# Performance work log

Measured on AMD Instinct MI355X. Metric: run time of the kernel, lower is better.

The kernel has to match this reference:

```python
import jax, jax.numpy as jnp
import numpy as np

H2 = 512  # 2 * hidden_dim
B, TK = 64, 2048


def setup_inputs() -> dict:
    key = jax.random.key(0)
    ks = jax.random.split(key, 10)
    s_t_hat = jax.random.normal(ks[0], (B, H2), dtype=jnp.float32)
    encoder_outputs = jax.random.normal(ks[1], (B, TK, H2), dtype=jnp.float32)
    encoder_feature = jax.random.normal(ks[2], (B, TK, H2), dtype=jnp.float32)
    enc_padding_mask = jnp.ones((B, TK), dtype=jnp.float32)
    coverage = jax.random.uniform(ks[3], (B, TK), dtype=jnp.float32)
    # learned params (torch Linear stores W as [out, in]; we keep math explicit)
    sc = 1.0 / np.sqrt(H2)
    W_dp = jax.random.uniform(ks[4], (H2, H2), minval=-sc, maxval=sc, dtype=jnp.float32)  # decode_proj weight [out,in]
    b_dp = jax.random.uniform(ks[5], (H2,), minval=-sc, maxval=sc, dtype=jnp.float32)
    W_c = jax.random.uniform(ks[6], (H2,), minval=-1.0, maxval=1.0, dtype=jnp.float32)  # Linear(1, 2H) weight, squeezed
    v_w = jax.random.uniform(ks[7], (H2,), minval=-sc, maxval=sc, dtype=jnp.float32)  # Linear(2H, 1) weight
    v_b = jax.random.uniform(ks[8], (), minval=-sc, maxval=sc, dtype=jnp.float32)
    return {
        "s_t_hat": s_t_hat,
        "encoder_outputs": encoder_outputs,
        "encoder_feature": encoder_feature,
        "enc_padding_mask": enc_padding_mask,
        "coverage": coverage,
        "W_dp": W_dp,
        "b_dp": b_dp,
        "W_c": W_c,
        "v_w": v_w,
        "v_b": v_b,
    }


def reference(s_t_hat, encoder_outputs, encoder_feature, enc_padding_mask, coverage,
              W_dp, b_dp, W_c, v_w, v_b):
    # decoder projection: [b, n]
    dec_fea = s_t_hat @ W_dp.T + b_dp
    # broadcast add over t_k, plus coverage feature (Linear(1, 2H) == outer product)
    att_features = encoder_feature + dec_fea[:, None, :] + coverage[:, :, None] * W_c  # [b, t_k, n]
    e = jnp.tanh(att_features)
    scores = jnp.einsum('btn,n->bt', e, v_w) + v_b  # [b, t_k]
    attn_ = jax.nn.softmax(scores, axis=1) * enc_padding_mask
    attn = attn_ / jnp.sum(attn_, axis=1, keepdims=True)  # renormalized [b, t_k]
    c_t = jnp.einsum('bt,btn->bn', attn, encoder_outputs)  # [b, n]
    coverage_new = coverage + attn
    return (c_t, attn, coverage_new)
```

## Files before the change

kernel.cpp:

```cpp
#include <hip/hip_runtime.h>
#include <math.h>

#define H2 512
#define NB 64
#define TK 2048
#define SPLIT 16

#define LOG2E 1.44269504088896f
#define TWO_LOG2E 2.88539008177793f

__global__ __launch_bounds__(256) void k_decproj(const float* __restrict__ s,
                                                 const float* __restrict__ W,
                                                 const float* __restrict__ bias,
                                                 float* __restrict__ dec) {
    const int bb = blockIdx.x;
    const int wave = threadIdx.x >> 6;
    const int lane = threadIdx.x & 63;
    const float* srow = s + bb * H2;
    float4 s0 = *(const float4*)(srow + lane * 8);
    float4 s1 = *(const float4*)(srow + lane * 8 + 4);
    #pragma unroll
    for (int i = 0; i < 8; ++i) {
        const int n = blockIdx.y * 32 + wave * 8 + i;
        const float* wrow = W + (size_t)n * H2;
        float4 w0 = *(const float4*)(wrow + lane * 8);
        float4 w1 = *(const float4*)(wrow + lane * 8 + 4);
        float acc = s0.x * w0.x + s0.y * w0.y + s0.z * w0.z + s0.w * w0.w +
                    s1.x * w1.x + s1.y * w1.y + s1.z * w1.z + s1.w * w1.w;
        #pragma unroll
        for (int off = 1; off < 64; off <<= 1) acc += __shfl_xor(acc, off, 64);
        if (lane == 0) dec[bb * H2 + n] = acc + bias[n];
    }
}

__global__ __launch_bounds__(256) void k_scores(const float* __restrict__ ef,
                                                const float* __restrict__ dec,
                                                const float* __restrict__ cov,
                                                const float* __restrict__ wc,
                                                const float* __restrict__ vw,
                                                const float* __restrict__ vbp,
                                                float* __restrict__ scores) {
    const int bb = blockIdx.y;
    const int wave = threadIdx.x >> 6;
    const int lane = threadIdx.x & 63;
    const int n0 = lane * 8;

    float4 d0 = *(const float4*)(dec + bb * H2 + n0);
    float4 d1 = *(const float4*)(dec + bb * H2 + n0 + 4);
    float4 c0 = *(const float4*)(wc + n0);
    float4 c1 = *(const float4*)(wc + n0 + 4);
    float4 v0 = *(const float4*)(vw + n0);
    float4 v1 = *(const float4*)(vw + n0 + 4);

    float vwsum = v0.x + v0.y + v0.z + v0.w + v1.x + v1.y + v1.z + v1.w;
    #pragma unroll
    for (int off = 1; off < 64; off <<= 1) vwsum += __shfl_xor(vwsum, off, 64);

    v0.x *= -2.f; v0.y *= -2.f; v0.z *= -2.f; v0.w *= -2.f;
    v1.x *= -2.f; v1.y *= -2.f; v1.z *= -2.f; v1.w *= -2.f;
    const float vb = vbp[0];

    const int t0 = blockIdx.x * 16;
    for (int r = wave; r < 16; r += 4) {
        const int t = t0 + r;
        const size_t base = ((size_t)bb * TK + t) * H2;
        float4 e0 = *(const float4*)(ef + base + n0);
        float4 e1 = *(const float4*)(ef + base + n0 + 4);
        const float covt = cov[bb * TK + t];

        #define TERM(E, D, C, V) \
            ((V) * __builtin_amdgcn_rcpf(__builtin_amdgcn_exp2f(((E) + (D) + covt * (C)) * TWO_LOG2E) + 1.0f))
        float acc = TERM(e0.x, d0.x, c0.x, v0.x) + TERM(e0.y, d0.y, c0.y, v0.y) +
                    TERM(e0.z, d0.z, c0.z, v0.z) + TERM(e0.w, d0.w, c0.w, v0.w) +
                    TERM(e1.x, d1.x, c1.x, v1.x) + TERM(e1.y, d1.y, c1.y, v1.y) +
                    TERM(e1.z, d1.z, c1.z, v1.z) + TERM(e1.w, d1.w, c1.w, v1.w);
        #undef TERM

        #pragma unroll
        for (int off = 1; off < 64; off <<= 1) acc += __shfl_xor(acc, off, 64);
        if (lane == 0) scores[bb * TK + t] = vwsum + acc + vb;
    }
}

__global__ __launch_bounds__(256) void k_softmax(float* __restrict__ attn,
                                                 const float* __restrict__ mask,
                                                 const float* __restrict__ cov,
                                                 float* __restrict__ covnew) {
    const int bb = blockIdx.x;
    const int tid = threadIdx.x;
    const int lane = tid & 63, wave = tid >> 6;
    float s[8], mk[8];
    float m = -1e30f;
    #pragma unroll
    for (int i = 0; i < 8; ++i) {
        const int t = tid + i * 256;
        s[i] = attn[bb * TK + t];
        mk[i] = mask[bb * TK + t];
        m = fmaxf(m, s[i]);
    }
    #pragma unroll
    for (int off = 1; off < 64; off <<= 1) m = fmaxf(m, __shfl_xor(m, off, 64));
    __shared__ float redm[4], reds[4];
    if (lane == 0) redm[wave] = m;
    __syncthreads();
    m = fmaxf(fmaxf(redm[0], redm[1]), fmaxf(redm[2], redm[3]));

    float e[8];
    float sum = 0.f;
    #pragma unroll
    for (int i = 0; i < 8; ++i) {
        e[i] = __builtin_amdgcn_exp2f((s[i] - m) * LOG2E) * mk[i];
        sum += e[i];
    }
    #pragma unroll
    for (int off = 1; off < 64; off <<= 1) sum += __shfl_xor(sum, off, 64);
    if (lane == 0) reds[wave] = sum;
    __syncthreads();
    sum = reds[0] + reds[1] + reds[2] + reds[3];
    const float inv = 1.0f / sum;

    #pragma unroll
    for (int i = 0; i < 8; ++i) {
        const int t = tid + i * 256;
        const float a = e[i] * inv;
        attn[bb * TK + t] = a;
        covnew[bb * TK + t] = cov[bb * TK + t] + a;
    }
}

__global__ __launch_bounds__(256) void k_ct_part(const float* __restrict__ eo,
                                                 const float* __restrict__ attn,
                                                 float* __restrict__ part) {
    const int bb = blockIdx.y, sp = blockIdx.x;
    const int tid = threadIdx.x;
    const int ng = tid & 127, th = tid >> 7;
    const int t0 = sp * (TK / SPLIT);
    float4 acc = make_float4(0.f, 0.f, 0.f, 0.f);
    for (int t = t0 + th; t < t0 + (TK / SPLIT); t += 2) {
        const float a = attn[bb * TK + t];
        const float4 v = *((const float4*)(eo + ((size_t)bb * TK + t) * H2) + ng);
        acc.x += a * v.x; acc.y += a * v.y; acc.z += a * v.z; acc.w += a * v.w;
    }
    __shared__ float4 lds[128];
    if (th) lds[ng] = acc;
    __syncthreads();
    if (!th) {
        const float4 o = lds[ng];
        acc.x += o.x; acc.y += o.y; acc.z += o.z; acc.w += o.w;
        *(float4*)(part + ((size_t)(bb * SPLIT + sp)) * H2 + ng * 4) = acc;
    }
}

__global__ __launch_bounds__(512) void k_ct_final(const float* __restrict__ part,
                                                  float* __restrict__ ct) {
    const int bb = blockIdx.x, n = threadIdx.x;
    float acc = 0.f;
    #pragma unroll
    for (int sp = 0; sp < SPLIT; ++sp) acc += part[((size_t)(bb * SPLIT + sp)) * H2 + n];
    ct[bb * H2 + n] = acc;
}

extern "C" void kernel_launch(void* const* d_in, const int* in_sizes, int n_in,
                              void* d_out, int out_size, void* d_ws, size_t ws_size,
                              hipStream_t stream) {
    const float* s_t_hat  = (const float*)d_in[0];
    const float* enc_out  = (const float*)d_in[1];
    const float* enc_feat = (const float*)d_in[2];
    const float* mask     = (const float*)d_in[3];
    const float* cov      = (const float*)d_in[4];
    const float* W_dp     = (const float*)d_in[5];
    const float* b_dp     = (const float*)d_in[6];
    const float* W_c      = (const float*)d_in[7];
    const float* v_w      = (const float*)d_in[8];
    const float* v_b      = (const float*)d_in[9];

    float* out = (float*)d_out;
    float* ct     = out;
    float* attn   = out + NB * H2;
    float* covnew = attn + NB * TK;

    float* dec  = (float*)d_ws;
    float* part = dec + NB * H2;

    k_decproj<<<dim3(NB, 16), 256, 0, stream>>>(s_t_hat, W_dp, b_dp, dec);
    k_scores<<<dim3(TK / 16, NB), 256, 0, stream>>>(enc_feat, dec, cov, W_c, v_w, v_b, attn);
    k_softmax<<<NB, 256, 0, stream>>>(attn, mask, cov, covnew);
    k_ct_part<<<dim3(SPLIT, NB), 256, 0, stream>>>(enc_out, attn, part);
    k_ct_final<<<NB, 512, 0, stream>>>(part, ct);
}
```

Measured before the change: 113.9 us.

## Fuse score computation with context accumulation using unnormalized softmax weights

Merges the scores, softmax and context-partial kernels into one kernel per time tile. It computes exp(score)*mask without max subtraction, keeps the weights in LDS, and immediately accumulates the weighted encoder_outputs into per-tile partials. Normalization is deferred: one small kernel computes the sum, attn and coverage, and another reduces the partials and scales them by the inverse sum. This removes launches and attn round trips and overlaps the tanh-heavy score work with streaming encoder_outputs. Dropping the max subtraction relies on scores staying bounded, which tanh and the small v_w make true here but which is less robust in general.

```diff
diff --git a/kernel.cpp b/kernel.cpp
--- a/kernel.cpp
+++ b/kernel.cpp
@@ -4,7 +4,6 @@
 #define H2 512
 #define NB 64
 #define TK 2048
-#define SPLIT 16
 
 #define LOG2E 1.44269504088896f
 #define TWO_LOG2E 2.88539008177793f
@@ -33,17 +32,26 @@
     }
 }
 
-__global__ __launch_bounds__(256) void k_scores(const float* __restrict__ ef,
-                                                const float* __restrict__ dec,
-                                                const float* __restrict__ cov,
-                                                const float* __restrict__ wc,
-                                                const float* __restrict__ vw,
-                                                const float* __restrict__ vbp,
-                                                float* __restrict__ scores) {
+template <int TILE>
+__global__ __launch_bounds__(256) void k_fused(const float* __restrict__ ef,
+                                               const float* __restrict__ eo,
+                                               const float* __restrict__ dec,
+                                               const float* __restrict__ cov,
+                                               const float* __restrict__ mask,
+                                               const float* __restrict__ wc,
+                                               const float* __restrict__ vw,
+                                               const float* __restrict__ vbp,
+                                               float* __restrict__ w,
+                                               float* __restrict__ part) {
     const int bb = blockIdx.y;
-    const int wave = threadIdx.x >> 6;
-    const int lane = threadIdx.x & 63;
+    const int sp = blockIdx.x;
+    const int t0 = sp * TILE;
+    const int tid = threadIdx.x;
+    const int wave = tid >> 6, lane = tid & 63;
     const int n0 = lane * 8;
+
+    __shared__ float e_lds[TILE];
+    __shared__ float4 red[128];
 
     float4 d0 = *(const float4*)(dec + bb * H2 + n0);
     float4 d1 = *(const float4*)(dec + bb * H2 + n0 + 4);
@@ -56,108 +64,120 @@
     #pragma unroll
     for (int off = 1; off < 64; off <<= 1) vwsum += __shfl_xor(vwsum, off, 64);
 
+    d0.x *= TWO_LOG2E; d0.y *= TWO_LOG2E; d0.z *= TWO_LOG2E; d0.w *= TWO_LOG2E;
+    d1.x *= TWO_LOG2E; d1.y *= TWO_LOG2E; d1.z *= TWO_LOG2E; d1.w *= TWO_LOG2E;
+    c0.x *= TWO_LOG2E; c0.y *= TWO_LOG2E; c0.z *= TWO_LOG2E; c0.w *= TWO_LOG2E;
+    c1.x *= TWO_LOG2E; c1.y *= TWO_LOG2E; c1.z *= TWO_LOG2E; c1.w *= TWO_LOG2E;
     v0.x *= -2.f; v0.y *= -2.f; v0.z *= -2.f; v0.w *= -2.f;
     v1.x *= -2.f; v1.y *= -2.f; v1.z *= -2.f; v1.w *= -2.f;
     const float vb = vbp[0];
 
-    const int t0 = blockIdx.x * 16;
-    for (int r = wave; r < 16; r += 4) {
-        const int t = t0 + r;
-        const size_t base = ((size_t)bb * TK + t) * H2;
-        float4 e0 = *(const float4*)(ef + base + n0);
-        float4 e1 = *(const float4*)(ef + base + n0 + 4);
-        const float covt = cov[bb * TK + t];
-
-        #define TERM(E, D, C, V) \
-            ((V) * __builtin_amdgcn_rcpf(__builtin_amdgcn_exp2f(((E) + (D) + covt * (C)) * TWO_LOG2E) + 1.0f))
-        float acc = TERM(e0.x, d0.x, c0.x, v0.x) + TERM(e0.y, d0.y, c0.y, v0.y) +
-                    TERM(e0.z, d0.z, c0.z, v0.z) + TERM(e0.w, d0.w, c0.w, v0.w) +
-                    TERM(e1.x, d1.x, c1.x, v1.x) + TERM(e1.y, d1.y, c1.y, v1.y) +
-                    TERM(e1.z, d1.z, c1.z, v1.z) + TERM(e1.w, d1.w, c1.w, v1.w);
-        #undef TERM
-
+    constexpr int R = TILE / 4;
+    #pragma unroll
+    for (int j0 = 0; j0 < R; j0 += 4) {
+        float4 ea[4][2];
+        float cv4[4], mk4[4];
         #pragma unroll
-        for (int off = 1; off < 64; off <<= 1) acc += __shfl_xor(acc, off, 64);
-        if (lane == 0) scores[bb * TK + t] = vwsum + acc + vb;
-    }
-}
-
-__global__ __launch_bounds__(256) void k_softmax(float* __restrict__ attn,
-                                                 const float* __restrict__ mask,
-                                                 const float* __restrict__ cov,
-                                                 float* __restrict__ covnew) {
+        for (int i = 0; i < 4; ++i) {
+            const int t = t0 + wave + 4 * (j0 + i);
+            const float* p = ef + ((size_t)bb * TK + t) * H2 + n0;
+            ea[i][0] = *(const float4*)p;
+            ea[i][1] = *(const float4*)(p + 4);
+            cv4[i] = cov[bb * TK + t];
+            mk4[i] = mask[bb * TK + t];
+        }
+        #pragma unroll
+        for (int i = 0; i < 4; ++i) {
+            const float cv = cv4[i];
+            #define TERM(E, D, C, V) \
+                ((V) * __builtin_amdgcn_rcpf(__builtin_amdgcn_exp2f(fmaf((E), TWO_LOG2E, fmaf(cv, (C), (D)))) + 1.0f))
+            float acc = TERM(ea[i][0].x, d0.x, c0.x, v0.x) + TERM(ea[i][0].y, d0.y, c0.y, v0.y) +
+                        TERM(ea[i][0].z, d0.z, c0.z, v0.z) + TERM(ea[i][0].w, d0.w, c0.w, v0.w) +
+                        TERM(ea[i][1].x, d1.x, c1.x, v1.x) + TERM(ea[i][1].y, d1.y, c1.y, v1.y) +
+                        TERM(ea[i][1].z, d1.z, c1.z, v1.z) + TERM(ea[i][1].w, d1.w, c1.w, v1.w);
+            #undef TERM
+            #pragma unroll
+            for (int off = 1; off < 64; off <<= 1) acc += __shfl_xor(acc, off, 64);
+            if (lane == 0) {
+                const int r = wave + 4 * (j0 + i);
+                const float score = vwsum + acc + vb;
+                const float e = __builtin_amdgcn_exp2f(score * LOG2E) * mk4[i];
+                e_lds[r] = e;
+                w[bb * TK + t0 + r] = e;
+            }
+        }
+    }
+    __syncthreads();
+
+    const int ng = tid & 127, th = tid >> 7;
+    float4 acc = make_float4(0.f, 0.f, 0.f, 0.f);
+    #pragma unroll 8
+    for (int i = 0; i < TILE / 2; ++i) {
+        const int r = th + 2 * i;
+        const float a = e_lds[r];
+        const float4 vv = *((const float4*)(eo + ((size_t)bb * TK + t0 + r) * H2) + ng);
+        acc.x = fmaf(a, vv.x, acc.x);
+        acc.y = fmaf(a, vv.y, acc.y);
+        acc.z = fmaf(a, vv.z, acc.z);
+        acc.w = fmaf(a, vv.w, acc.w);
+    }
+    if (th) red[ng] = acc;
+    __syncthreads();
+    if (!th) {
+        const float4 o = red[ng];
+        acc.x += o.x; acc.y += o.y; acc.z += o.z; acc.w += o.w;
+        *(float4*)(part + ((size_t)bb * (TK / TILE) + sp) * H2 + ng * 4) = acc;
+    }
+}
+
+__global__ __launch_bounds__(256) void k_finA(const float* __restrict__ w,
+                                              const float* __restrict__ cov,
+                                              float* __restrict__ attn,
+                                              float* __restrict__ covnew,
+                                              float* __restrict__ invs) {
     const int bb = blockIdx.x;
     const int tid = threadIdx.x;
     const int lane = tid & 63, wave = tid >> 6;
-    float s[8], mk[8];
-    float m = -1e30f;
+    float v[8];
+    float sum = 0.f;
     #pragma unroll
     for (int i = 0; i < 8; ++i) {
-        const int t = tid + i * 256;
-        s[i] = attn[bb * TK + t];
-        mk[i] = mask[bb * TK + t];
-        m = fmaxf(m, s[i]);
-    }
-    #pragma unroll
-    for (int off = 1; off < 64; off <<= 1) m = fmaxf(m, __shfl_xor(m, off, 64));
-    __shared__ float redm[4], reds[4];
-    if (lane == 0) redm[wave] = m;
-    __syncthreads();
-    m = fmaxf(fmaxf(redm[0], redm[1]), fmaxf(redm[2], redm[3]));
-
-    float e[8];
-    float sum = 0.f;
-    #pragma unroll
-    for (int i = 0; i < 8; ++i) {
-        e[i] = __builtin_amdgcn_exp2f((s[i] - m) * LOG2E) * mk[i];
-        sum += e[i];
+        v[i] = w[bb * TK + tid + 256 * i];
+        sum += v[i];
     }
     #pragma unroll
     for (int off = 1; off < 64; off <<= 1) sum += __shfl_xor(sum, off, 64);
+    __shared__ float reds[4];
     if (lane == 0) reds[wave] = sum;
     __syncthreads();
     sum = reds[0] + reds[1] + reds[2] + reds[3];
     const float inv = 1.0f / sum;
-
     #pragma unroll
     for (int i = 0; i < 8; ++i) {
-        const int t = tid + i * 256;
-        const float a = e[i] * inv;
+        const int t = tid + 256 * i;
+        const float a = v[i] * inv;
         attn[bb * TK + t] = a;
         covnew[bb * TK + t] = cov[bb * TK + t] + a;
     }
-}
-
-__global__ __launch_bounds__(256) void k_ct_part(const float* __restrict__ eo,
-                                                 const float* __restrict__ attn,
-                                                 float* __restrict__ part) {
-    const int bb = blockIdx.y, sp = blockIdx.x;
+    if (tid == 0) invs[bb] = inv;
+}
+
+template <int SPLIT>
+__global__ __launch_bounds__(128) void k_finB(const float* __restrict__ part,
+                                              const float* __restrict__ invs,
+                                              float* __restrict__ ct) {
+    const int bb = blockIdx.x;
     const int tid = threadIdx.x;
-    const int ng = tid & 127, th = tid >> 7;
-    const int t0 = sp * (TK / SPLIT);
     float4 acc = make_float4(0.f, 0.f, 0.f, 0.f);
-    for (int t = t0 + th; t < t0 + (TK / SPLIT); t += 2) {
-        const float a = attn[bb * TK + t];
-        const float4 v = *((const float4*)(eo + ((size_t)bb * TK + t) * H2) + ng);
-        acc.x += a * v.x; acc.y += a * v.y; acc.z += a * v.z; acc.w += a * v.w;
-    }
-    __shared__ float4 lds[128];
-    if (th) lds[ng] = acc;
-    __syncthreads();
-    if (!th) {
-        const float4 o = lds[ng];
-        acc.x += o.x; acc.y += o.y; acc.z += o.z; acc.w += o.w;
-        *(float4*)(part + ((size_t)(bb * SPLIT + sp)) * H2 + ng * 4) = acc;
-    }
-}
-
-__global__ __launch_bounds__(512) void k_ct_final(const float* __restrict__ part,
-                                                  float* __restrict__ ct) {
-    const int bb = blockIdx.x, n = threadIdx.x;
-    float acc = 0.f;
-    #pragma unroll
-    for (int sp = 0; sp < SPLIT; ++sp) acc += part[((size_t)(bb * SPLIT + sp)) * H2 + n];
-    ct[bb * H2 + n] = acc;
+    #pragma unroll 8
+    for (int sp = 0; sp < SPLIT; ++sp) {
+        const float4 p = *((const float4*)(part + ((size_t)bb * SPLIT + sp) * H2) + tid);
+        acc.x += p.x; acc.y += p.y; acc.z += p.z; acc.w += p.w;
+    }
+    const float inv = invs[bb];
+    float4 o;
+    o.x = acc.x * inv; o.y = acc.y * inv; o.z = acc.z * inv; o.w = acc.w * inv;
+    *(float4*)(ct + bb * H2 + tid * 4) = o;
 }
 
 extern "C" void kernel_launch(void* const* d_in, const int* in_sizes, int n_in,
@@ -180,11 +200,31 @@
     float* covnew = attn + NB * TK;
 
     float* dec  = (float*)d_ws;
-    float* part = dec + NB * H2;
+    float* w    = dec + NB * H2;
+    float* invs = w + NB * TK;
+    float* part = invs + 256;
+
+    const size_t base_floats = (size_t)NB * H2 + (size_t)NB * TK + 256;
+    auto need = [&](int tile) {
+        return (base_floats + (size_t)NB * (TK / tile) * H2) * sizeof(float);
+    };
 
     k_decproj<<<dim3(NB, 16), 256, 0, stream>>>(s_t_hat, W_dp, b_dp, dec);
-    k_scores<<<dim3(TK / 16, NB), 256, 0, stream>>>(enc_feat, dec, cov, W_c, v_w, v_b, attn);
-    k_softmax<<<NB, 256, 0, stream>>>(attn, mask, cov, covnew);
-    k_ct_part<<<dim3(SPLIT, NB), 256, 0, stream>>>(enc_out, attn, part);
-    k_ct_final<<<NB, 512, 0, stream>>>(part, ct);
-}
+
+    if (ws_size >= need(32)) {
+        k_fused<32><<<dim3(TK / 32, NB), 256, 0, stream>>>(enc_feat, enc_out, dec, cov, mask,
+                                                           W_c, v_w, v_b, w, part);
+        k_finA<<<NB, 256, 0, stream>>>(w, cov, attn, covnew, invs);
+        k_finB<TK / 32><<<NB, 128, 0, stream>>>(part, invs, ct);
+    } else if (ws_size >= need(64)) {
+        k_fused<64><<<dim3(TK / 64, NB), 256, 0, stream>>>(enc_feat, enc_out, dec, cov, mask,
+                                                           W_c, v_w, v_b, w, part);
+        k_finA<<<NB, 256, 0, stream>>>(w, cov, attn, covnew, invs);
+        k_finB<TK / 64><<<NB, 128, 0, stream>>>(part, invs, ct);
+    } else {
+        k_fused<128><<<dim3(TK / 128, NB), 256, 0, stream>>>(enc_feat, enc_out, dec, cov, mask,
+                                                             W_c, v_w, v_b, w, part);
+        k_finA<<<NB, 256, 0, stream>>>(w, cov, attn, covnew, invs);
+        k_finB<TK / 128><<<NB, 128, 0, stream>>>(part, invs, ct);
+    }
+}
```

New measurement: 123.1 us. 8.1% more time.

## Defer softmax normalization and fuse it into the final context reduction

Applied to the files above, without the earlier changes.

Each score kernel block now writes unnormalized exponentials (exp(score)*mask) with no max subtraction, and the context vector is accumulated from these unnormalized weights. A final kernel computes the sum, normalizes attn, coverage and c_t, and replaces the separate softmax and final-reduce kernels. The score kernel loads 8 rows per batch to raise memory-level parallelism and reduces through LDS instead of per-row 64-lane shuffles. The ct partial loop is unrolled with vectorized weight loads. Dropping max subtraction risks overflow for large scores, and it relies on score magnitudes staying bounded, which holds here because tanh output and v_w are bounded.

```diff
diff --git a/kernel.cpp b/kernel.cpp
--- a/kernel.cpp
+++ b/kernel.cpp
@@ -5,6 +5,7 @@
 #define NB 64
 #define TK 2048
 #define SPLIT 16
+#define TROWS 128
 
 #define LOG2E 1.44269504088896f
 #define TWO_LOG2E 2.88539008177793f
@@ -33,17 +34,21 @@
     }
 }
 
-__global__ __launch_bounds__(256) void k_scores(const float* __restrict__ ef,
-                                                const float* __restrict__ dec,
-                                                const float* __restrict__ cov,
-                                                const float* __restrict__ wc,
-                                                const float* __restrict__ vw,
-                                                const float* __restrict__ vbp,
-                                                float* __restrict__ scores) {
+__global__ __launch_bounds__(512) void k_scores2(const float* __restrict__ ef,
+                                                 const float* __restrict__ cov,
+                                                 const float* __restrict__ mask,
+                                                 const float* __restrict__ dec,
+                                                 const float* __restrict__ wc,
+                                                 const float* __restrict__ vw,
+                                                 const float* __restrict__ vbp,
+                                                 float* __restrict__ w) {
     const int bb = blockIdx.y;
-    const int wave = threadIdx.x >> 6;
-    const int lane = threadIdx.x & 63;
+    const int t0 = blockIdx.x * TROWS;
+    const int tid = threadIdx.x;
+    const int wave = tid >> 6, lane = tid & 63;
     const int n0 = lane * 8;
+
+    __shared__ float pl[TROWS][68];
 
     float4 d0 = *(const float4*)(dec + bb * H2 + n0);
     float4 d1 = *(const float4*)(dec + bb * H2 + n0 + 4);
@@ -56,108 +61,126 @@
     #pragma unroll
     for (int off = 1; off < 64; off <<= 1) vwsum += __shfl_xor(vwsum, off, 64);
 
+    d0.x *= TWO_LOG2E; d0.y *= TWO_LOG2E; d0.z *= TWO_LOG2E; d0.w *= TWO_LOG2E;
+    d1.x *= TWO_LOG2E; d1.y *= TWO_LOG2E; d1.z *= TWO_LOG2E; d1.w *= TWO_LOG2E;
+    c0.x *= TWO_LOG2E; c0.y *= TWO_LOG2E; c0.z *= TWO_LOG2E; c0.w *= TWO_LOG2E;
+    c1.x *= TWO_LOG2E; c1.y *= TWO_LOG2E; c1.z *= TWO_LOG2E; c1.w *= TWO_LOG2E;
     v0.x *= -2.f; v0.y *= -2.f; v0.z *= -2.f; v0.w *= -2.f;
     v1.x *= -2.f; v1.y *= -2.f; v1.z *= -2.f; v1.w *= -2.f;
     const float vb = vbp[0];
 
-    const int t0 = blockIdx.x * 16;
-    for (int r = wave; r < 16; r += 4) {
+    #pragma unroll
+    for (int j0 = 0; j0 < 16; j0 += 8) {
+        float4 ea[8][2];
+        float cv8[8];
+        #pragma unroll
+        for (int i = 0; i < 8; ++i) {
+            const int r = wave * 16 + j0 + i;
+            const float* p = ef + ((size_t)bb * TK + t0 + r) * H2 + n0;
+            ea[i][0] = *(const float4*)p;
+            ea[i][1] = *(const float4*)(p + 4);
+            cv8[i] = cov[bb * TK + t0 + r];
+        }
+        #pragma unroll
+        for (int i = 0; i < 8; ++i) {
+            const float cv = cv8[i];
+            #define TERM(E, D, C, V) \
+                ((V) * __builtin_amdgcn_rcpf(__builtin_amdgcn_exp2f(fmaf((E), TWO_LOG2E, fmaf(cv, (C), (D)))) + 1.0f))
+            const float acc = TERM(ea[i][0].x, d0.x, c0.x, v0.x) + TERM(ea[i][0].y, d0.y, c0.y, v0.y) +
+                              TERM(ea[i][0].z, d0.z, c0.z, v0.z) + TERM(ea[i][0].w, d0.w, c0.w, v0.w) +
+                              TERM(ea[i][1].x, d1.x, c1.x, v1.x) + TERM(ea[i][1].y, d1.y, c1.y, v1.y) +
+                              TERM(ea[i][1].z, d1.z, c1.z, v1.z) + TERM(ea[i][1].w, d1.w, c1.w, v1.w);
+            #undef TERM
+            pl[wave * 16 + j0 + i][lane] = acc;
+        }
+    }
+    __syncthreads();
+
+    const int r = tid >> 2, q = tid & 3;
+    const float* prow = &pl[r][q * 16];
+    const float4 x0 = *(const float4*)(prow);
+    const float4 x1 = *(const float4*)(prow + 4);
+    const float4 x2 = *(const float4*)(prow + 8);
+    const float4 x3 = *(const float4*)(prow + 12);
+    float s = x0.x + x0.y + x0.z + x0.w + x1.x + x1.y + x1.z + x1.w +
+              x2.x + x2.y + x2.z + x2.w + x3.x + x3.y + x3.z + x3.w;
+    s += __shfl_xor(s, 1, 64);
+    s += __shfl_xor(s, 2, 64);
+    if (q == 0) {
         const int t = t0 + r;
-        const size_t base = ((size_t)bb * TK + t) * H2;
-        float4 e0 = *(const float4*)(ef + base + n0);
-        float4 e1 = *(const float4*)(ef + base + n0 + 4);
-        const float covt = cov[bb * TK + t];
-
-        #define TERM(E, D, C, V) \
-            ((V) * __builtin_amdgcn_rcpf(__builtin_amdgcn_exp2f(((E) + (D) + covt * (C)) * TWO_LOG2E) + 1.0f))
-        float acc = TERM(e0.x, d0.x, c0.x, v0.x) + TERM(e0.y, d0.y, c0.y, v0.y) +
-                    TERM(e0.z, d0.z, c0.z, v0.z) + TERM(e0.w, d0.w, c0.w, v0.w) +
-                    TERM(e1.x, d1.x, c1.x, v1.x) + TERM(e1.y, d1.y, c1.y, v1.y) +
-                    TERM(e1.z, d1.z, c1.z, v1.z) + TERM(e1.w, d1.w, c1.w, v1.w);
-        #undef TERM
-
-        #pragma unroll
-        for (int off = 1; off < 64; off <<= 1) acc += __shfl_xor(acc, off, 64);
-        if (lane == 0) scores[bb * TK + t] = vwsum + acc + vb;
-    }
-}
-
-__global__ __launch_bounds__(256) void k_softmax(float* __restrict__ attn,
-                                                 const float* __restrict__ mask,
-                                                 const float* __restrict__ cov,
-                                                 float* __restrict__ covnew) {
+        const float score = vwsum + s + vb;
+        w[bb * TK + t] = __builtin_amdgcn_exp2f(score * LOG2E) * mask[bb * TK + t];
+    }
+}
+
+__global__ __launch_bounds__(256) void k_ctpart(const float* __restrict__ eo,
+                                                const float* __restrict__ w,
+                                                float* __restrict__ part) {
+    const int bb = blockIdx.y, sp = blockIdx.x;
+    const int tid = threadIdx.x;
+    const int ng = tid & 127, th = tid >> 7;
+    const int t0 = sp * (TK / SPLIT) + th * 64;
+    const float* wp = w + bb * TK + t0;
+    const float4* ep = (const float4*)(eo + ((size_t)bb * TK + t0) * H2) + ng;
+
+    float4 acc = make_float4(0.f, 0.f, 0.f, 0.f);
+    #pragma unroll 2
+    for (int i0 = 0; i0 < 64; i0 += 4) {
+        const float4 a4 = *(const float4*)(wp + i0);
+        const float4 r0 = ep[(size_t)(i0 + 0) * 128];
+        const float4 r1 = ep[(size_t)(i0 + 1) * 128];
+        const float4 r2 = ep[(size_t)(i0 + 2) * 128];
+        const float4 r3 = ep[(size_t)(i0 + 3) * 128];
+        acc.x = fmaf(a4.x, r0.x, acc.x); acc.y = fmaf(a4.x, r0.y, acc.y);
+        acc.z = fmaf(a4.x, r0.z, acc.z); acc.w = fmaf(a4.x, r0.w, acc.w);
+        acc.x = fmaf(a4.y, r1.x, acc.x); acc.y = fmaf(a4.y, r1.y, acc.y);
+        acc.z = fmaf(a4.y, r1.z, acc.z); acc.w = fmaf(a4.y, r1.w, acc.w);
+        acc.x = fmaf(a4.z, r2.x, acc.x); acc.y = fmaf(a4.z, r2.y, acc.y);
+        acc.z = fmaf(a4.z, r2.z, acc.z); acc.w = fmaf(a4.z, r2.w, acc.w);
+        acc.x = fmaf(a4.w, r3.x, acc.x); acc.y = fmaf(a4.w, r3.y, acc.y);
+        acc.z = fmaf(a4.w, r3.z, acc.z); acc.w = fmaf(a4.w, r3.w, acc.w);
+    }
+    __shared__ float4 red[128];
+    if (th) red[ng] = acc;
+    __syncthreads();
+    if (!th) {
+        const float4 o = red[ng];
+        acc.x += o.x; acc.y += o.y; acc.z += o.z; acc.w += o.w;
+        *(float4*)(part + ((size_t)bb * SPLIT + sp) * H2 + ng * 4) = acc;
+    }
+}
+
+__global__ __launch_bounds__(512) void k_finish(const float* __restrict__ w,
+                                                const float* __restrict__ cov,
+                                                const float* __restrict__ part,
+                                                float* __restrict__ attn,
+                                                float* __restrict__ covnew,
+                                                float* __restrict__ ct) {
     const int bb = blockIdx.x;
     const int tid = threadIdx.x;
     const int lane = tid & 63, wave = tid >> 6;
-    float s[8], mk[8];
-    float m = -1e30f;
-    #pragma unroll
-    for (int i = 0; i < 8; ++i) {
-        const int t = tid + i * 256;
-        s[i] = attn[bb * TK + t];
-        mk[i] = mask[bb * TK + t];
-        m = fmaxf(m, s[i]);
-    }
-    #pragma unroll
-    for (int off = 1; off < 64; off <<= 1) m = fmaxf(m, __shfl_xor(m, off, 64));
-    __shared__ float redm[4], reds[4];
-    if (lane == 0) redm[wave] = m;
+
+    const float4 w4 = *(const float4*)(w + bb * TK + tid * 4);
+    float s = w4.x + w4.y + w4.z + w4.w;
+    #pragma unroll
+    for (int off = 1; off < 64; off <<= 1) s += __shfl_xor(s, off, 64);
+    __shared__ float rs[8];
+    if (lane == 0) rs[wave] = s;
     __syncthreads();
-    m = fmaxf(fmaxf(redm[0], redm[1]), fmaxf(redm[2], redm[3]));
-
-    float e[8];
-    float sum = 0.f;
-    #pragma unroll
-    for (int i = 0; i < 8; ++i) {
-        e[i] = __builtin_amdgcn_exp2f((s[i] - m) * LOG2E) * mk[i];
-        sum += e[i];
-    }
-    #pragma unroll
-    for (int off = 1; off < 64; off <<= 1) sum += __shfl_xor(sum, off, 64);
-    if (lane == 0) reds[wave] = sum;
-    __syncthreads();
-    sum = reds[0] + reds[1] + reds[2] + reds[3];
-    const float inv = 1.0f / sum;
-
-    #pragma unroll
-    for (int i = 0; i < 8; ++i) {
-        const int t = tid + i * 256;
-        const float a = e[i] * inv;
-        attn[bb * TK + t] = a;
-        covnew[bb * TK + t] = cov[bb * TK + t] + a;
-    }
-}
-
-__global__ __launch_bounds__(256) void k_ct_part(const float* __restrict__ eo,
-                                                 const float* __restrict__ attn,
-                                                 float* __restrict__ part) {
-    const int bb = blockIdx.y, sp = blockIdx.x;
-    const int tid = threadIdx.x;
-    const int ng = tid & 127, th = tid >> 7;
-    const int t0 = sp * (TK / SPLIT);
-    float4 acc = make_float4(0.f, 0.f, 0.f, 0.f);
-    for (int t = t0 + th; t < t0 + (TK / SPLIT); t += 2) {
-        const float a = attn[bb * TK + t];
-        const float4 v = *((const float4*)(eo + ((size_t)bb * TK + t) * H2) + ng);
-        acc.x += a * v.x; acc.y += a * v.y; acc.z += a * v.z; acc.w += a * v.w;
-    }
-    __shared__ float4 lds[128];
-    if (th) lds[ng] = acc;
-    __syncthreads();
-    if (!th) {
-        const float4 o = lds[ng];
-        acc.x += o.x; acc.y += o.y; acc.z += o.z; acc.w += o.w;
-        *(float4*)(part + ((size_t)(bb * SPLIT + sp)) * H2 + ng * 4) = acc;
-    }
-}
-
-__global__ __launch_bounds__(512) void k_ct_final(const float* __restrict__ part,
-                                                  float* __restrict__ ct) {
-    const int bb = blockIdx.x, n = threadIdx.x;
+    s = rs[0] + rs[1] + rs[2] + rs[3] + rs[4] + rs[5] + rs[6] + rs[7];
+    const float inv = 1.0f / s;
+
+    const float4 c4 = *(const float4*)(cov + bb * TK + tid * 4);
+    float4 a4, n4;
+    a4.x = w4.x * inv; a4.y = w4.y * inv; a4.z = w4.z * inv; a4.w = w4.w * inv;
+    n4.x = c4.x + a4.x; n4.y = c4.y + a4.y; n4.z = c4.z + a4.z; n4.w = c4.w + a4.w;
+    *(float4*)(attn + bb * TK + tid * 4) = a4;
+    *(float4*)(covnew + bb * TK + tid * 4) = n4;
+
     float acc = 0.f;
     #pragma unroll
-    for (int sp = 0; sp < SPLIT; ++sp) acc += part[((size_t)(bb * SPLIT + sp)) * H2 + n];
-    ct[bb * H2 + n] = acc;
+    for (int sp = 0; sp < SPLIT; ++sp) acc += part[((size_t)bb * SPLIT + sp) * H2 + tid];
+    ct[bb * H2 + tid] = acc * inv;
 }
 
 extern "C" void kernel_launch(void* const* d_in, const int* in_sizes, int n_in,
@@ -180,11 +203,11 @@
     float* covnew = attn + NB * TK;
 
     float* dec  = (float*)d_ws;
-    float* part = dec + NB * H2;
+    float* w    = dec + NB * H2;
+    float* part = w + NB * TK;
 
     k_decproj<<<dim3(NB, 16), 256, 0, stream>>>(s_t_hat, W_dp, b_dp, dec);
-    k_scores<<<dim3(TK / 16, NB), 256, 0, stream>>>(enc_feat, dec, cov, W_c, v_w, v_b, attn);
-    k_softmax<<<NB, 256, 0, stream>>>(attn, mask, cov, covnew);
-    k_ct_part<<<dim3(SPLIT, NB), 256, 0, stream>>>(enc_out, attn, part);
-    k_ct_final<<<NB, 512, 0, stream>>>(part, ct);
-}
+    k_scores2<<<dim3(TK / TROWS, NB), 512, 0, stream>>>(enc_feat, cov, mask, dec, W_c, v_w, v_b, w);
+    k_ctpart<<<dim3(SPLIT, NB), 256, 0, stream>>>(enc_out, w, part);
+    k_finish<<<NB, 512, 0, stream>>>(w, cov, part, attn, covnew, ct);
+}
```

New measurement: 118.6 us. +4.1%, slower.
